# Performance work log

Hardware: AMD Instinct MI355X
Metric: run time of the kernel (lower is better)

## Reference

```python
import jax, jax.numpy as jnp
import numpy as np

B = 32; H = 56; W = 56; C = 384; NH = 12; WS = 14; SS = 7
L = H * W; N = WS * WS; HD = C // NH; SCALE = HD ** -0.5; HID = 4 * C
NW = (H // WS) * (W // WS)
EPS = 1e-5

def _relative_index():
    ch = np.arange(WS)[:, None].repeat(WS, 1)
    cw = np.arange(WS)[None, :].repeat(WS, 0)
    coords = np.stack([ch, cw], -1).reshape(-1, 2)  # [N,2]
    rel = coords[:, None, :] - coords[None, :, :]
    rel = rel + (WS - 1)
    rel[:, :, 0] *= 2 * WS - 1
    return rel.sum(-1)  # [N,N], values in [0,(2WS-1)^2)

def _attn_mask():
    img = np.zeros((H, W))
    sl = (slice(0, -WS), slice(-WS, -SS), slice(-SS, None))
    cnt = 0
    for hs in sl:
        for ws_ in sl:
            img[hs, ws_] = cnt; cnt += 1
    mw = img.reshape(H // WS, WS, W // WS, WS).transpose(0, 2, 1, 3).reshape(-1, N)
    am = mw[:, None, :] - mw[:, :, None]  # [nW,N,N]
    return np.where(am != 0, -100.0, 0.0).astype(np.float32)

REL_IDX = jnp.asarray(_relative_index())
MASK = jnp.asarray(_attn_mask())  # [NW,N,N]

def _ln(x, w, b):
    m = jnp.mean(x, -1, keepdims=True)
    v = jnp.mean((x - m) ** 2, -1, keepdims=True)
    return (x - m) * jax.lax.rsqrt(v + EPS) * w + b

def setup_inputs() -> dict:
    key = jax.random.key(0)
    ks = jax.random.split(key, 8)
    s = 0.02
    return {
        "x": jax.random.normal(ks[0], (B, L, C), jnp.float32),
        "norm1_w": jnp.ones((C,), jnp.float32),
        "norm1_b": jnp.zeros((C,), jnp.float32),
        "qkv_w": jax.random.normal(ks[1], (3 * C, C), jnp.float32) * s,
        "qkv_b": jnp.zeros((3 * C,), jnp.float32),
        "proj_w": jax.random.normal(ks[2], (C, C), jnp.float32) * s,
        "proj_b": jnp.zeros((C,), jnp.float32),
        "relative_table": jax.random.normal(ks[3], ((2 * WS - 1) ** 2, 2 * NH), jnp.float32) * s,
        "norm2_w": jnp.ones((C,), jnp.float32),
        "norm2_b": jnp.zeros((C,), jnp.float32),
        "fc1_w": jax.random.normal(ks[4], (HID, C), jnp.float32) * s,
        "fc1_b": jnp.zeros((HID,), jnp.float32),
        "fc2_w": jax.random.normal(ks[5], (C, HID), jnp.float32) * s,
        "fc2_b": jnp.zeros((C,), jnp.float32),
    }

def reference(x, norm1_w, norm1_b, qkv_w, qkv_b, proj_w, proj_b,
              relative_table, norm2_w, norm2_b, fc1_w, fc1_b, fc2_w, fc2_b):
    shortcut = x
    xn = _ln(x, norm1_w, norm1_b).reshape(B, H, W, C)
    # cyclic shift + window partition -> [B*NW, N, C]
    xs = jnp.roll(xn, (-SS, -SS), (1, 2))
    xw = xs.reshape(B, H // WS, WS, W // WS, WS, C).transpose(0, 1, 3, 2, 4, 5).reshape(-1, N, C)
    B_ = B * NW
    qkv = (xw @ qkv_w.T + qkv_b).reshape(B_, N, 3, NH, HD).transpose(2, 0, 3, 1, 4)
    q, k, v = qkv[0] * SCALE, qkv[1], qkv[2]  # [B_,NH,N,HD]
    attn = jnp.einsum('bhnd,bhmd->bhnm', q, k)  # [B_,NH,N,N]
    rel = relative_table[REL_IDX]  # [N,N,2*NH]
    rel = rel.transpose(2, 0, 1)  # [2*NH,N,N]
    bias, rscale = rel[:NH], rel[NH:]
    attn = attn + bias[None]
    attn = attn.reshape(B, NW, NH, N, N) + MASK[None, :, None]
    attn = jax.nn.softmax(attn.reshape(B_, NH, N, N), axis=-1)
    attn = attn * rscale[None]  # multiplicative relative scale AFTER softmax
    out = jnp.einsum('bhnm,bhmd->bhnd', attn, v)
    out = out.transpose(0, 2, 1, 3).reshape(B_, N, C)
    out = out @ proj_w.T + proj_b
    # window reverse + reverse shift
    xr = out.reshape(B, H // WS, W // WS, WS, WS, C).transpose(0, 1, 3, 2, 4, 5).reshape(B, H, W, C)
    xr = jnp.roll(xr, (SS, SS), (1, 2)).reshape(B, L, C)
    x = shortcut + xr
    h = _ln(x, norm2_w, norm2_b)
    h = jax.nn.gelu(h @ fc1_w.T + fc1_b, approximate=False) @ fc2_w.T + fc2_b
    return x + h
```

## Files before the change

### kernel.cpp

```cpp
#include <hip/hip_runtime.h>
#include <hip/hip_bf16.h>
#include <math.h>

#define BDIM 32
#define HDIM 56
#define WDIM 56
#define CDIM 384
#define NHEAD 12
#define WSZ 14
#define SSZ 7
#define LDIM (HDIM*WDIM)
#define NTOK (WSZ*WSZ)
#define HDHEAD (CDIM/NHEAD)
#define HIDDIM (4*CDIM)
#define NWIN 16
#define BWIN (BDIM*NWIN)
#define MROWS (BDIM*LDIM)
#define EPSLN 1e-5f
#define ATTSCALE 0.17677669529663687f
#define QKVC (3*CDIM)

#define KROW 40
#define VROW 232
#define PROW 232

typedef __hip_bfloat16 bf16;
typedef __attribute__((ext_vector_type(8))) short bf16x8;
typedef __attribute__((ext_vector_type(4))) short s16x4;
typedef __attribute__((ext_vector_type(2))) short s16x2;
typedef __attribute__((ext_vector_type(4))) float f32x4;

#define ASYNC16(gp, lp) __builtin_amdgcn_global_load_lds( \
    (__attribute__((address_space(1))) void*)(gp),        \
    (__attribute__((address_space(3))) void*)(lp), 16, 0, 0)

static __device__ __forceinline__ short f2bfs(float x) {
  union { bf16 h; short s; } u; u.h = __float2bfloat16(x); return u.s;
}
static __device__ __forceinline__ float bfs2f(short s) {
  unsigned int u = ((unsigned int)(unsigned short)s) << 16;
  float f; __builtin_memcpy(&f, &u, 4); return f;
}

__global__ __launch_bounds__(256) void k_cvt(const float* __restrict__ in,
                                             bf16* __restrict__ out, int n)
{
  int i = blockIdx.x * 256 + threadIdx.x;
  if (i < n) out[i] = __float2bfloat16(in[i]);
}

template<bool WIN, typename TIN>
__global__ __launch_bounds__(256) void k_ln(const TIN* __restrict__ xin,
    const float* __restrict__ gw, const float* __restrict__ gb,
    bf16* __restrict__ out)
{
  int lane = threadIdx.x & 63, wid = threadIdx.x >> 6;
  int r = blockIdx.x*4 + wid;
  const TIN* xp = xin + (size_t)r * CDIM;
  float v[6];
  if constexpr (sizeof(TIN) == 4) {
    float4 a = *(const float4*)((const float*)xp + lane*4);
    float2 b = *(const float2*)((const float*)xp + 256 + lane*2);
    v[0]=a.x; v[1]=a.y; v[2]=a.z; v[3]=a.w; v[4]=b.x; v[5]=b.y;
  } else {
    s16x4 a = *(const s16x4*)((const short*)xp + lane*4);
    s16x2 b = *(const s16x2*)((const short*)xp + 256 + lane*2);
    v[0]=bfs2f(a[0]); v[1]=bfs2f(a[1]); v[2]=bfs2f(a[2]); v[3]=bfs2f(a[3]);
    v[4]=bfs2f(b[0]); v[5]=bfs2f(b[1]);
  }
  float s = 0.f, ss = 0.f;
  #pragma unroll
  for (int j = 0; j < 6; j++) { s += v[j]; ss += v[j]*v[j]; }
  #pragma unroll
  for (int o = 1; o < 64; o <<= 1) { s += __shfl_xor(s, o); ss += __shfl_xor(ss, o); }
  float mean = s * (1.0f/CDIM);
  float var  = ss * (1.0f/CDIM) - mean*mean;
  float rstd = rsqrtf(var + EPSLN);

  size_t orow;
  if (WIN) {
    int b = r / LDIM, l = r % LDIM;
    int h = l / WDIM, w = l % WDIM;
    int h2 = (h + HDIM - SSZ) % HDIM, w2 = (w + WDIM - SSZ) % WDIM;
    int wh = h2 / WSZ, ii = h2 % WSZ, ww = w2 / WSZ, jj = w2 % WSZ;
    int b_ = b*NWIN + wh*4 + ww;
    int n  = ii*WSZ + jj;
    orow = ((size_t)b_*NTOK + n) * CDIM;
  } else {
    orow = (size_t)r * CDIM;
  }
  float4 w4 = *(const float4*)(gw + lane*4);
  float2 w2 = *(const float2*)(gw + 256 + lane*2);
  float4 g4 = *(const float4*)(gb + lane*4);
  float2 g2 = *(const float2*)(gb + 256 + lane*2);
  s16x4 o4;
  o4[0] = f2bfs((v[0]-mean)*rstd*w4.x + g4.x);
  o4[1] = f2bfs((v[1]-mean)*rstd*w4.y + g4.y);
  o4[2] = f2bfs((v[2]-mean)*rstd*w4.z + g4.z);
  o4[3] = f2bfs((v[3]-mean)*rstd*w4.w + g4.w);
  *(s16x4*)((short*)out + orow + lane*4) = o4;
  s16x2 o2;
  o2[0] = f2bfs((v[4]-mean)*rstd*w2.x + g2.x);
  o2[1] = f2bfs((v[5]-mean)*rstd*w2.y + g2.y);
  *(s16x2*)((short*)out + orow + 256 + lane*2) = o2;
}

template<int KD, int EPI>
__global__ __launch_bounds__(512, 4) void k_mgemm(
    const bf16* __restrict__ A, const bf16* __restrict__ Wb,
    const float* __restrict__ bias, const float* __restrict__ aux,
    const bf16* __restrict__ auxb,
    float* __restrict__ outf, bf16* __restrict__ outb, int gx)
{
  __shared__ short As[2][256*32];
  __shared__ short Bs[2][128*32];
  int tid  = threadIdx.x;
  int lane = tid & 63, wid = tid >> 6;
  int c15 = lane & 15, h4 = lane >> 4;
  int wr = wid >> 1, wc = wid & 1;

  int nwg = gridDim.x, bid = blockIdx.x;
  int swz = (bid & 7) * (nwg >> 3) + (bid >> 3);
  int ty = swz / gx, tx = swz - ty * gx;
  int row0 = ty * 256, col0 = tx * 128;

  f32x4 acc[4][4] = {};

  int r0  = tid >> 2, b0 = tid & 3;
  int sk0 = (b0 ^ (r0 & 3) ^ ((r0 >> 2) & 3)) * 8;

  const int NT = KD / 32;

#define STAGE_T(k0, bf) do { \
    ASYNC16(A  + (size_t)(row0 + r0)*KD       + (k0) + sk0, &As[bf][tid*8]); \
    ASYNC16(A  + (size_t)(row0 + r0 + 128)*KD + (k0) + sk0, &As[bf][(tid+512)*8]); \
    ASYNC16(Wb + (size_t)(col0 + r0)*KD       + (k0) + sk0, &Bs[bf][tid*8]); \
  } while (0)

  STAGE_T(0, 0);

  int rblk = (h4 ^ (c15 & 3) ^ ((c15 >> 2) & 3)) * 8;

  for (int t = 0; t < NT; t++) {
    int cur = t & 1;
    if (t + 1 < NT) {
      STAGE_T((t+1)*32, cur^1);
      asm volatile("s_waitcnt vmcnt(3)" ::: "memory");
    } else {
      asm volatile("s_waitcnt vmcnt(0)" ::: "memory");
    }
    __builtin_amdgcn_s_barrier();
    __builtin_amdgcn_sched_barrier(0);

    bf16x8 af[4], bfr[4];
    #pragma unroll
    for (int m = 0; m < 4; m++)
      af[m] = *reinterpret_cast<const bf16x8*>(&As[cur][(wr*64 + m*16 + c15)*32 + rblk]);
    #pragma unroll
    for (int n = 0; n < 4; n++)
      bfr[n] = *reinterpret_cast<const bf16x8*>(&Bs[cur][(wc*64 + n*16 + c15)*32 + rblk]);
    #pragma unroll
    for (int n = 0; n < 4; n++)
      #pragma unroll
      for (int m = 0; m < 4; m++)
        acc[n][m] = __builtin_amdgcn_mfma_f32_16x16x32_bf16(bfr[n], af[m], acc[n][m], 0, 0, 0);

    __builtin_amdgcn_sched_barrier(0);
    __builtin_amdgcn_s_barrier();
  }
#undef STAGE_T

  int rb = row0 + wr*64 + c15;
  int cb = col0 + wc*64 + h4*4;
  #pragma unroll
  for (int m = 0; m < 4; m++) {
    int r = rb + m*16;
    if constexpr (EPI == 0) {
      #pragma unroll
      for (int n = 0; n < 4; n++) {
        int c0 = cb + n*16;
        f32x4 v = acc[n][m];
        f32x4 b4 = *(const f32x4*)&bias[c0];
        float scl = (c0 < CDIM) ? ATTSCALE : 1.f;
        s16x4 o;
        #pragma unroll
        for (int i = 0; i < 4; i++) o[i] = f2bfs((v[i] + b4[i]) * scl);
        *(s16x4*)&outb[(size_t)r*QKVC + c0] = o;
      }
    } else if constexpr (EPI == 1) {
      int b_ = r / NTOK, nn = r % NTOK;
      int b = b_ >> 4, wi = b_ & 15, wh = wi >> 2, ww = wi & 3;
      int ii = nn / WSZ, jj = nn % WSZ;
      int hh = (wh*WSZ + ii + SSZ) % HDIM;
      int wcc = (ww*WSZ + jj + SSZ) % WDIM;
      size_t rr = ((size_t)b*LDIM + hh*WDIM + wcc) * CDIM;
      #pragma unroll
      for (int n = 0; n < 4; n++) {
        int c0 = cb + n*16;
        f32x4 v = acc[n][m];
        f32x4 b4 = *(const f32x4*)&bias[c0];
        f32x4 a4 = *(const f32x4*)&aux[rr + c0];
        s16x4 o;
        #pragma unroll
        for (int i = 0; i < 4; i++) o[i] = f2bfs(a4[i] + v[i] + b4[i]);
        *(s16x4*)&outb[rr + c0] = o;
      }
    } else if constexpr (EPI == 2) {
      #pragma unroll
      for (int n = 0; n < 4; n++) {
        int c0 = cb + n*16;
        f32x4 v = acc[n][m];
        f32x4 b4 = *(const f32x4*)&bias[c0];
        s16x4 o;
        #pragma unroll
        for (int i = 0; i < 4; i++) {
          float val = v[i] + b4[i];
          val = 0.5f * val * (1.0f + erff(val * 0.70710678118654752f));
          o[i] = f2bfs(val);
        }
        *(s16x4*)&outb[(size_t)r*HIDDIM + c0] = o;
      }
    } else {
      #pragma unroll
      for (int n = 0; n < 4; n++) {
        int c0 = cb + n*16;
        f32x4 v = acc[n][m];
        f32x4 b4 = *(const f32x4*)&bias[c0];
        s16x4 ab = *(const s16x4*)&auxb[(size_t)r*CDIM + c0];
        f32x4 o;
        #pragma unroll
        for (int i = 0; i < 4; i++) o[i] = v[i] + b4[i] + bfs2f(ab[i]);
        *(f32x4*)&outf[(size_t)r*CDIM + c0] = o;
      }
    }
  }
}

__global__ __launch_bounds__(256) void k_attn_mfma(const bf16* __restrict__ qkv,
    const float* __restrict__ rt, bf16* __restrict__ out)
{
  __shared__ short  Ks[208*KROW];
  __shared__ short  Vt[32*VROW];
  __shared__ short  Ps[4][16*PROW];
  __shared__ float2 tab2[729];
  __shared__ int    regv[208];

  int blk = blockIdx.x;
  int b_ = blk / NHEAD, head = blk % NHEAD;
  int tid = threadIdx.x, lane = tid & 63, wid = tid >> 6;
  int c15 = lane & 15, h4 = lane >> 4;

  const bf16* rowbase = qkv + (size_t)b_*NTOK*QKVC + head*HDHEAD;
  const bf16* kp = rowbase + CDIM;
  const bf16* vp = rowbase + 2*CDIM;
  for (int c = tid; c < 784; c += 256) {
    int m = c >> 2, k8 = (c & 3) * 8;
    *(bf16x8*)&Ks[m*KROW + k8] = *(const bf16x8*)(kp + (size_t)m*QKVC + k8);
    bf16x8 vv = *(const bf16x8*)(vp + (size_t)m*QKVC + k8);
    #pragma unroll
    for (int j = 0; j < 8; j++) Vt[(k8+j)*VROW + m] = vv[j];
  }
  for (int e = tid; e < 12*KROW; e += 256) Ks[196*KROW + e] = 0;
  for (int e = tid; e < 32*28; e += 256) Vt[(e/28)*VROW + 196 + (e%28)] = 0;
  for (int e = tid; e < 729; e += 256)
    tab2[e] = make_float2(rt[e*2*NHEAD + head], rt[e*2*NHEAD + NHEAD + head]);
  {
    int wi = b_ & 15, wh = wi >> 2, ww = wi & 3;
    for (int e = tid; e < 208; e += 256) {
      int rv = 0;
      if (e < NTOK) {
        int i = e / WSZ, j = e % WSZ;
        int ha = wh*WSZ + i, wa = ww*WSZ + j;
        int rh = ha < (HDIM-WSZ) ? 0 : (ha < (HDIM-SSZ) ? 1 : 2);
        int rw = wa < (WDIM-WSZ) ? 0 : (wa < (WDIM-SSZ) ? 1 : 2);
        rv = rh*3 + rw;
      }
      regv[e] = rv;
    }
  }
  __syncthreads();

  int   moff[13], mreg[13];
  float mpad[13];
  #pragma unroll
  for (int t = 0; t < 13; t++) {
    int m  = t*16 + c15;
    int mm = min(m, NTOK-1);
    moff[t] = (mm/WSZ)*27 + (mm%WSZ);
    mreg[t] = regv[mm];
    mpad[t] = (m >= NTOK) ? -1e30f : 0.f;
  }

  short* myP = &Ps[wid][0];
  #pragma unroll
  for (int i = 0; i < 4; i++) myP[(h4*4+i)*PROW + 208 + c15] = 0;

  bf16* op = out + (size_t)b_*NTOK*CDIM + head*HDHEAD;

  for (int s = wid; s < 13; s += 4) {
    int qrow = min(s*16 + c15, NTOK-1);
    bf16x8 qf = *(const bf16x8*)(rowbase + (size_t)qrow*QKVC + h4*8);

    f32x4 sc[13];
    #pragma unroll
    for (int t = 0; t < 13; t++) {
      bf16x8 kf = *(const bf16x8*)&Ks[(t*16 + c15)*KROW + h4*8];
      sc[t] = __builtin_amdgcn_mfma_f32_16x16x32_bf16(qf, kf, (f32x4){0.f,0.f,0.f,0.f}, 0, 0, 0);
    }

    #pragma unroll
    for (int i = 0; i < 4; i++) {
      int n  = s*16 + h4*4 + i;
      int nc = min(n, NTOK-1);
      int nbase = ((nc/WSZ) + 13)*27 + (nc%WSZ) + 13;
      int nreg  = regv[nc];
      float rr[13];
      float sum = 0.f;
      #pragma unroll
      for (int t = 0; t < 13; t++) {
        float2 hr = tab2[nbase - moff[t]];
        float sv = sc[t][i] + hr.x + ((mreg[t] != nreg) ? -100.f : 0.f) + mpad[t];
        float e = __expf(sv);
        rr[t] = hr.y;
        sc[t][i] = e; sum += e;
      }
      #pragma unroll
      for (int o = 1; o < 16; o <<= 1) sum += __shfl_xor(sum, o);
      float inv = 1.f / sum;
      int prow = h4*4 + i;
      #pragma unroll
      for (int t = 0; t < 13; t++)
        myP[prow*PROW + t*16 + c15] = f2bfs(sc[t][i] * inv * rr[t]);
    }

    asm volatile("s_waitcnt lgkmcnt(0)" ::: "memory");
    __builtin_amdgcn_sched_barrier(0);

    f32x4 o0 = {0.f,0.f,0.f,0.f}, o1 = {0.f,0.f,0.f,0.f};
    #pragma unroll
    for (int t7 = 0; t7 < 7; t7++) {
      bf16x8 pf = *(const bf16x8*)&myP[c15*PROW + t7*32 + h4*8];
      bf16x8 v0 = *(const bf16x8*)&Vt[c15*VROW + t7*32 + h4*8];
      bf16x8 v1 = *(const bf16x8*)&Vt[(16 + c15)*VROW + t7*32 + h4*8];
      o0 = __builtin_amdgcn_mfma_f32_16x16x32_bf16(pf, v0, o0, 0, 0, 0);
      o1 = __builtin_amdgcn_mfma_f32_16x16x32_bf16(pf, v1, o1, 0, 0, 0);
    }

    #pragma unroll
    for (int i = 0; i < 4; i++) {
      int n = s*16 + h4*4 + i;
      if (n < NTOK) {
        op[(size_t)n*CDIM + c15]      = __float2bfloat16(o0[i]);
        op[(size_t)n*CDIM + 16 + c15] = __float2bfloat16(o1[i]);
      }
    }
  }
}

extern "C" void kernel_launch(void* const* d_in, const int* in_sizes, int n_in,
                              void* d_out, int out_size, void* d_ws, size_t ws_size,
                              hipStream_t stream)
{
  const float* x      = (const float*)d_in[0];
  const float* n1w    = (const float*)d_in[1];
  const float* n1b    = (const float*)d_in[2];
  const float* qkv_w  = (const float*)d_in[3];
  const float* qkv_b  = (const float*)d_in[4];
  const float* proj_w = (const float*)d_in[5];
  const float* proj_b = (const float*)d_in[6];
  const float* rt     = (const float*)d_in[7];
  const float* n2w    = (const float*)d_in[8];
  const float* n2b    = (const float*)d_in[9];
  const float* fc1_w  = (const float*)d_in[10];
  const float* fc1_b  = (const float*)d_in[11];
  const float* fc2_w  = (const float*)d_in[12];
  const float* fc2_b  = (const float*)d_in[13];

  char* ws = (char*)d_ws;
  const size_t SZ_BF = (size_t)MROWS * CDIM * 2;
  bf16*  xw      = (bf16*)ws;
  bf16*  attnout = (bf16*)ws;
  bf16*  qkv     = (bf16*)(ws + SZ_BF);
  bf16*  x2b     = (bf16*)(ws + SZ_BF);
  bf16*  hln     = (bf16*)(ws + 2*SZ_BF);
  bf16*  hid     = (bf16*)(ws + 4*SZ_BF);
  const int NQKVW = 3*CDIM*CDIM;
  const int NPROJW = CDIM*CDIM;
  const int NFCW  = HIDDIM*CDIM;
  bf16* wq  = (bf16*)(ws + 4*SZ_BF);
  bf16* wp  = wq + NQKVW;
  bf16* wf1 = (bf16*)ws;
  bf16* wf2 = wf1 + NFCW;

  k_cvt<<<(NQKVW+255)/256, 256, 0, stream>>>(qkv_w, wq, NQKVW);
  k_cvt<<<(NPROJW+255)/256, 256, 0, stream>>>(proj_w, wp, NPROJW);

  k_ln<true, float><<<MROWS/4, 256, 0, stream>>>(x, n1w, n1b, xw);
  k_mgemm<CDIM, 0><<<(MROWS/256)*9, 512, 0, stream>>>(
      xw, wq, qkv_b, nullptr, nullptr, nullptr, qkv, 9);
  k_attn_mfma<<<BWIN*NHEAD, 256, 0, stream>>>(qkv, rt, attnout);
  k_mgemm<CDIM, 1><<<(MROWS/256)*3, 512, 0, stream>>>(
      attnout, wp, proj_b, x, nullptr, nullptr, x2b, 3);

  k_cvt<<<(NFCW+255)/256, 256, 0, stream>>>(fc1_w, wf1, NFCW);
  k_cvt<<<(NFCW+255)/256, 256, 0, stream>>>(fc2_w, wf2, NFCW);

  k_ln<false, bf16><<<MROWS/4, 256, 0, stream>>>(x2b, n2w, n2b, hln);
  k_mgemm<CDIM, 2><<<(MROWS/256)*12, 512, 0, stream>>>(
      hln, wf1, fc1_b, nullptr, nullptr, nullptr, hid, 12);
  k_mgemm<HIDDIM, 3><<<(MROWS/256)*3, 512, 0, stream>>>(
      hid, wf2, fc2_b, nullptr, x2b, (float*)d_out, nullptr, 3);
}
```

Baseline: 1.012 ms.

## Keep softmax probabilities in registers by transposing the attention MFMA layout

The QK^T MFMA now swaps its operands so each lane holds the scores for one query column. The softmax result can then feed the PV product directly from registers through 16x16x16 MFMAs, with no round trip through the per-wave P buffer in shared memory, its wait, or its scheduling barrier. Region IDs and relative offsets are computed in registers, so the regv table is gone, and launch bounds request higher occupancy. In exchange the PV step issues twice as many smaller MFMAs, runs extra scalar index arithmetic per element, and adds register pressure.

```diff
diff --git a/kernel.cpp b/kernel.cpp
--- a/kernel.cpp
+++ b/kernel.cpp
@@ -22,13 +22,18 @@
 
 #define KROW 40
 #define VROW 232
-#define PROW 232
 
 typedef __hip_bfloat16 bf16;
 typedef __attribute__((ext_vector_type(8))) short bf16x8;
 typedef __attribute__((ext_vector_type(4))) short s16x4;
 typedef __attribute__((ext_vector_type(2))) short s16x2;
 typedef __attribute__((ext_vector_type(4))) float f32x4;
+
+#if defined(__HIP_DEVICE_COMPILE__)
+#define MFMA16(a,b,c) __builtin_amdgcn_mfma_f32_16x16x16bf16_1k(a,b,c,0,0,0)
+#else
+#define MFMA16(a,b,c) (c)
+#endif
 
 #define ASYNC16(gp, lp) __builtin_amdgcn_global_load_lds( \
     (__attribute__((address_space(1))) void*)(gp),        \
@@ -236,14 +241,12 @@
   }
 }
 
-__global__ __launch_bounds__(256) void k_attn_mfma(const bf16* __restrict__ qkv,
+__global__ __launch_bounds__(256, 4) void k_attn_mfma(const bf16* __restrict__ qkv,
     const float* __restrict__ rt, bf16* __restrict__ out)
 {
   __shared__ short  Ks[208*KROW];
   __shared__ short  Vt[32*VROW];
-  __shared__ short  Ps[4][16*PROW];
   __shared__ float2 tab2[729];
-  __shared__ int    regv[208];
 
   int blk = blockIdx.x;
   int b_ = blk / NHEAD, head = blk % NHEAD;
@@ -264,95 +267,88 @@
   for (int e = tid; e < 32*28; e += 256) Vt[(e/28)*VROW + 196 + (e%28)] = 0;
   for (int e = tid; e < 729; e += 256)
     tab2[e] = make_float2(rt[e*2*NHEAD + head], rt[e*2*NHEAD + NHEAD + head]);
-  {
-    int wi = b_ & 15, wh = wi >> 2, ww = wi & 3;
-    for (int e = tid; e < 208; e += 256) {
-      int rv = 0;
-      if (e < NTOK) {
-        int i = e / WSZ, j = e % WSZ;
-        int ha = wh*WSZ + i, wa = ww*WSZ + j;
-        int rh = ha < (HDIM-WSZ) ? 0 : (ha < (HDIM-SSZ) ? 1 : 2);
-        int rw = wa < (WDIM-WSZ) ? 0 : (wa < (WDIM-SSZ) ? 1 : 2);
-        rv = rh*3 + rw;
-      }
-      regv[e] = rv;
-    }
-  }
   __syncthreads();
 
-  int   moff[13], mreg[13];
-  float mpad[13];
+  int wi = b_ & 15, wh = wi >> 2, ww = wi & 3;
+  int whb = wh*WSZ, wwb = ww*WSZ;
+
+  int encv[13], mregp[13];
   #pragma unroll
   for (int t = 0; t < 13; t++) {
-    int m  = t*16 + c15;
-    int mm = min(m, NTOK-1);
-    moff[t] = (mm/WSZ)*27 + (mm%WSZ);
-    mreg[t] = regv[mm];
-    mpad[t] = (m >= NTOK) ? -1e30f : 0.f;
-  }
-
-  short* myP = &Ps[wid][0];
-  #pragma unroll
-  for (int i = 0; i < 4; i++) myP[(h4*4+i)*PROW + 208 + c15] = 0;
+    int m0 = t*16 + h4*4;
+    int mi = m0 / 14, mj = m0 - (m0/14)*14;
+    encv[t] = (mi*27 + mj) | (mj << 16);
+    int rp = 0, mi2 = mi, mj2 = mj;
+    #pragma unroll
+    for (int i = 0; i < 4; i++) {
+      int ha = whb + mi2, wa = wwb + mj2;
+      int rr = (ha < 42 ? 0 : (ha < 49 ? 1 : 2))*3
+             + (wa < 42 ? 0 : (wa < 49 ? 1 : 2));
+      rp |= rr << (8*i);
+      mj2++; if (mj2 == 14) { mj2 = 0; mi2++; }
+    }
+    mregp[t] = rp;
+  }
 
   bf16* op = out + (size_t)b_*NTOK*CDIM + head*HDHEAD;
 
   for (int s = wid; s < 13; s += 4) {
-    int qrow = min(s*16 + c15, NTOK-1);
-    bf16x8 qf = *(const bf16x8*)(rowbase + (size_t)qrow*QKVC + h4*8);
+    int n = s*16 + c15;
+    int ncl = min(n, NTOK-1);
+    bf16x8 qf = *(const bf16x8*)(rowbase + (size_t)ncl*QKVC + h4*8);
 
     f32x4 sc[13];
     #pragma unroll
     for (int t = 0; t < 13; t++) {
       bf16x8 kf = *(const bf16x8*)&Ks[(t*16 + c15)*KROW + h4*8];
-      sc[t] = __builtin_amdgcn_mfma_f32_16x16x32_bf16(qf, kf, (f32x4){0.f,0.f,0.f,0.f}, 0, 0, 0);
-    }
-
-    #pragma unroll
-    for (int i = 0; i < 4; i++) {
-      int n  = s*16 + h4*4 + i;
-      int nc = min(n, NTOK-1);
-      int nbase = ((nc/WSZ) + 13)*27 + (nc%WSZ) + 13;
-      int nreg  = regv[nc];
-      float rr[13];
-      float sum = 0.f;
-      #pragma unroll
-      for (int t = 0; t < 13; t++) {
-        float2 hr = tab2[nbase - moff[t]];
-        float sv = sc[t][i] + hr.x + ((mreg[t] != nreg) ? -100.f : 0.f) + mpad[t];
+      sc[t] = __builtin_amdgcn_mfma_f32_16x16x32_bf16(kf, qf, (f32x4){0.f,0.f,0.f,0.f}, 0, 0, 0);
+    }
+
+    int ni = ncl / 14, nj = ncl - (ncl/14)*14;
+    int nbase = (ni + 13)*27 + nj + 13;
+    int nreg = ((whb + ni) < 42 ? 0 : ((whb + ni) < 49 ? 1 : 2))*3
+             + ((wwb + nj) < 42 ? 0 : ((wwb + nj) < 49 ? 1 : 2));
+
+    float sum = 0.f;
+    #pragma unroll
+    for (int t = 0; t < 13; t++) {
+      int moff = encv[t] & 0xFFFF, mj = encv[t] >> 16;
+      int rp = mregp[t];
+      #pragma unroll
+      for (int i = 0; i < 4; i++) {
+        int idx = nbase - moff; idx = idx < 0 ? 0 : idx;
+        float2 hr = tab2[idx];
+        float sv = sc[t][i] + hr.x;
+        if (((rp >> (8*i)) & 255) != nreg) sv -= 100.f;
+        if (t == 12 && (h4*4 + i) >= 4) sv = -1e30f;
         float e = __expf(sv);
-        rr[t] = hr.y;
-        sc[t][i] = e; sum += e;
+        sum += e;
+        sc[t][i] = e * hr.y;
+        mj++; bool w = (mj == 14); moff += w ? 14 : 1; mj = w ? 0 : mj;
       }
-      #pragma unroll
-      for (int o = 1; o < 16; o <<= 1) sum += __shfl_xor(sum, o);
-      float inv = 1.f / sum;
-      int prow = h4*4 + i;
-      #pragma unroll
-      for (int t = 0; t < 13; t++)
-        myP[prow*PROW + t*16 + c15] = f2bfs(sc[t][i] * inv * rr[t]);
-    }
-
-    asm volatile("s_waitcnt lgkmcnt(0)" ::: "memory");
-    __builtin_amdgcn_sched_barrier(0);
+    }
+    sum += __shfl_xor(sum, 16);
+    sum += __shfl_xor(sum, 32);
+    float inv = 1.f / sum;
 
     f32x4 o0 = {0.f,0.f,0.f,0.f}, o1 = {0.f,0.f,0.f,0.f};
     #pragma unroll
-    for (int t7 = 0; t7 < 7; t7++) {
-      bf16x8 pf = *(const bf16x8*)&myP[c15*PROW + t7*32 + h4*8];
-      bf16x8 v0 = *(const bf16x8*)&Vt[c15*VROW + t7*32 + h4*8];
-      bf16x8 v1 = *(const bf16x8*)&Vt[(16 + c15)*VROW + t7*32 + h4*8];
-      o0 = __builtin_amdgcn_mfma_f32_16x16x32_bf16(pf, v0, o0, 0, 0, 0);
-      o1 = __builtin_amdgcn_mfma_f32_16x16x32_bf16(pf, v1, o1, 0, 0, 0);
-    }
-
-    #pragma unroll
-    for (int i = 0; i < 4; i++) {
-      int n = s*16 + h4*4 + i;
-      if (n < NTOK) {
-        op[(size_t)n*CDIM + c15]      = __float2bfloat16(o0[i]);
-        op[(size_t)n*CDIM + 16 + c15] = __float2bfloat16(o1[i]);
-      }
+    for (int t = 0; t < 13; t++) {
+      s16x4 pf;
+      #pragma unroll
+      for (int i = 0; i < 4; i++) pf[i] = f2bfs(sc[t][i] * inv);
+      s16x4 va = *(const s16x4*)&Vt[c15*VROW + t*16 + h4*4];
+      s16x4 vb = *(const s16x4*)&Vt[(16 + c15)*VROW + t*16 + h4*4];
+      o0 = MFMA16(va, pf, o0);
+      o1 = MFMA16(vb, pf, o1);
+    }
+
+    if (n < NTOK) {
+      s16x4 w0, w1;
+      #pragma unroll
+      for (int i = 0; i < 4; i++) { w0[i] = f2bfs(o0[i]); w1[i] = f2bfs(o1[i]); }
+      *(s16x4*)((short*)op + (size_t)n*CDIM + h4*4)      = w0;
+      *(s16x4*)((short*)op + (size_t)n*CDIM + 16 + h4*4) = w1;
     }
   }
 }
```

New measurement: 2.340 ms. 131% more time.
